# Kernel tuning notes

Hardware: AMD Instinct MI355X
Metric: run time of the kernel (lower is better)

## Reference

```python
import jax, jax.numpy as jnp
import numpy as np

EPS = 1e-4
N_ITERS = 3


def setup_inputs() -> dict:
    key = jax.random.key(0)
    k1, k2, k3, k4 = jax.random.split(key, 4)
    B, M, T, D = 8, 64, 256, 64
    M_emb = jax.random.normal(k1, (B, M, D), dtype=jnp.float32)
    Ht_n = jax.random.normal(k2, (B, T, D), dtype=jnp.float32)
    new_M_emb_init = jax.random.uniform(k3, (B, M, D), dtype=jnp.float32)
    # learned bilinear routing weights, scaled to keep exp(b) in range
    W = jax.random.normal(k4, (M, M + T, D, D), dtype=jnp.float32) * 0.01
    return {"M_emb": M_emb, "Ht_n": Ht_n, "new_M_emb_init": new_M_emb_init, "W": W}


def reference(M_emb, Ht_n, new_M_emb_init, W):
    # cat_emb: [B, M+T, D]
    cat_emb = jnp.concatenate([M_emb, Ht_n], axis=1)
    # Loop-invariant projection: u[b,i,t,d] = sum_k W[i,t,d,k] * cat_emb[b,t,k]
    # (both routing einsums contract W with cat_emb identically)
    u = jnp.einsum('itdk,btk->bitd', W, cat_emb)  # [B, M, M+T, D]
    m = new_M_emb_init  # [B, M, D]
    for _ in range(N_ITERS):
        b = jnp.einsum('bid,bitd->bit', m, u)          # routing logits
        alph = jax.nn.softmax(b, axis=-1)              # exp(b)/sum_t exp(b)
        s = jnp.tanh(jnp.einsum('bit,bitd->bid', alph, u))
        n = jnp.linalg.norm(s, axis=-1, keepdims=True) + EPS
        m = (n * n) / (1.0 + n * n) * (s / n)          # squash
    return m
```

## Files before the change

kernel.cpp:

```cpp
#include <hip/hip_runtime.h>

#define Bdim 8
#define Mdim 64
#define Tdim 256
#define MTdim 320
#define Ddim 64
#define EPSF 1e-4f

__device__ __forceinline__ void load_lds16(const void* g, void* l) {
    __builtin_amdgcn_global_load_lds(
        (const __attribute__((address_space(1))) void*)g,
        (__attribute__((address_space(3))) void*)l, 16, 0, 0);
}

__global__ __launch_bounds__(256) void u_kernel(
    const float* __restrict__ M_emb,
    const float* __restrict__ Ht,
    const float* __restrict__ W,
    float* __restrict__ u,
    int i0, int icap)
{
    const int t   = blockIdx.x;
    const int ii  = blockIdx.y;
    const int i   = i0 + ii;
    const int tid = (int)threadIdx.x;
    const int l   = tid & 63;
    const int w   = __builtin_amdgcn_readfirstlane(tid >> 6);

    __shared__ __align__(16) float wtile[64 * 64];
    __shared__ __align__(16) float catb[8 * 64];
    char* wl = (char*)wtile;
    char* cl = (char*)catb;

#pragma unroll
    for (int c = 0; c < 2; ++c) {
        const int b = 4 * c + (l >> 4);
        const float* crow = (t < Mdim)
            ? (M_emb + (((size_t)b * Mdim + t) << 6))
            : (Ht   + (((size_t)b * Tdim + (t - Mdim)) << 6));
        load_lds16((const char*)crow + (((l & 15) ^ b) * 16), cl + c * 1024);
    }

    const char* wt = (const char*)(W + (((size_t)i * MTdim + t) << 12));
#pragma unroll
    for (int s = 0; s < 4; ++s) {
        const int r   = w * 16 + s * 4 + (l >> 4);
        const int src = r * 256 + (((l & 15) ^ (r & 7)) * 16);
        load_lds16(wt + src, wl + (w * 4096 + s * 1024));
    }

    asm volatile("s_waitcnt vmcnt(0)" ::: "memory");
    __builtin_amdgcn_sched_barrier(0);

    const int d   = w * 16 + (l >> 2);
    const int bp  = l & 3;
    const int wb  = d * 256;
    const int cb0 = bp * 256;
    const int cb1 = (bp + 4) * 256;

    float a0 = 0.0f, a1 = 0.0f;
#pragma unroll
    for (int k4 = 0; k4 < 16; ++k4) {
        const float4 w4 = *reinterpret_cast<const float4*>(wl + wb  + ((k4 ^ (d & 7)) * 16));
        const float4 p  = *reinterpret_cast<const float4*>(cl + cb0 + ((k4 ^ bp) * 16));
        const float4 q  = *reinterpret_cast<const float4*>(cl + cb1 + ((k4 ^ (bp + 4)) * 16));
        a0 = fmaf(w4.x, p.x, a0); a0 = fmaf(w4.y, p.y, a0);
        a0 = fmaf(w4.z, p.z, a0); a0 = fmaf(w4.w, p.w, a0);
        a1 = fmaf(w4.x, q.x, a1); a1 = fmaf(w4.y, q.y, a1);
        a1 = fmaf(w4.z, q.z, a1); a1 = fmaf(w4.w, q.w, a1);
    }

    u[((((size_t)bp      * icap + ii) * MTdim + t) << 6) + d] = a0;
    u[((((size_t)(bp + 4)* icap + ii) * MTdim + t) << 6) + d] = a1;
}

__device__ __forceinline__ float4 shfl_xor4(float4 v, int m) {
    float4 r;
    r.x = __shfl_xor(v.x, m, 64);
    r.y = __shfl_xor(v.y, m, 64);
    r.z = __shfl_xor(v.z, m, 64);
    r.w = __shfl_xor(v.w, m, 64);
    return r;
}
__device__ __forceinline__ float4 add4(float4 a, float4 b) {
    float4 r; r.x = a.x + b.x; r.y = a.y + b.y; r.z = a.z + b.z; r.w = a.w + b.w;
    return r;
}

__global__ __launch_bounds__(320) void iter_kernel(
    const float* __restrict__ u,
    const float* __restrict__ m_init,
    float* __restrict__ out,
    int i0, int icap)
{
    const int ii   = blockIdx.x;
    const int i    = i0 + ii;
    const int b    = blockIdx.y;
    const int tid  = (int)threadIdx.x;
    const int lane = tid & 63;
    const int w    = tid >> 6;

    const float* ub = u + ((((size_t)b * icap + ii) * MTdim) << 6);

    __shared__ __align__(16) float m_lds[Ddim];
    __shared__ float wmax[5], wsum[5];
    __shared__ float partial[5 * 64];

    float4 u4[16];
    {
        const float* row = ub + ((size_t)tid << 6);
#pragma unroll
        for (int k4 = 0; k4 < 16; ++k4)
            u4[k4] = *reinterpret_cast<const float4*>(row + (k4 << 2));
    }

    if (tid < Ddim)
        m_lds[tid] = m_init[(((size_t)b * Mdim + i) << 6) + tid];
    __syncthreads();

    for (int iter = 0; iter < 3; ++iter) {
        float bt = 0.0f;
#pragma unroll
        for (int k4 = 0; k4 < 16; ++k4) {
            float4 mv = *reinterpret_cast<const float4*>(&m_lds[k4 << 2]);
            bt = fmaf(u4[k4].x, mv.x, bt);
            bt = fmaf(u4[k4].y, mv.y, bt);
            bt = fmaf(u4[k4].z, mv.z, bt);
            bt = fmaf(u4[k4].w, mv.w, bt);
        }

        float mx = bt;
#pragma unroll
        for (int off = 1; off < 64; off <<= 1)
            mx = fmaxf(mx, __shfl_xor(mx, off, 64));
        if (lane == 0) wmax[w] = mx;
        __syncthreads();
        const float bmax = fmaxf(fmaxf(fmaxf(wmax[0], wmax[1]),
                                       fmaxf(wmax[2], wmax[3])), wmax[4]);

        const float e = expf(bt - bmax);

        float sm = e;
#pragma unroll
        for (int off = 1; off < 64; off <<= 1)
            sm += __shfl_xor(sm, off, 64);
        if (lane == 0) wsum[w] = sm;

        float4 c8[8];
#pragma unroll
        for (int jj = 0; jj < 8; ++jj) {
            const bool up = (lane & 32) != 0;
            float4 keep = up ? u4[jj + 8] : u4[jj];
            float4 give = up ? u4[jj] : u4[jj + 8];
            float4 g; g.x = give.x * e; g.y = give.y * e;
                      g.z = give.z * e; g.w = give.w * e;
            float4 r = shfl_xor4(g, 32);
            float4 o;
            o.x = fmaf(keep.x, e, r.x); o.y = fmaf(keep.y, e, r.y);
            o.z = fmaf(keep.z, e, r.z); o.w = fmaf(keep.w, e, r.w);
            c8[jj] = o;
        }
        float4 c4[4];
#pragma unroll
        for (int jj = 0; jj < 4; ++jj) {
            const bool up = (lane & 16) != 0;
            float4 keep = up ? c8[jj + 4] : c8[jj];
            float4 give = up ? c8[jj] : c8[jj + 4];
            c4[jj] = add4(keep, shfl_xor4(give, 16));
        }
        float4 c2[2];
#pragma unroll
        for (int jj = 0; jj < 2; ++jj) {
            const bool up = (lane & 8) != 0;
            float4 keep = up ? c4[jj + 2] : c4[jj];
            float4 give = up ? c4[jj] : c4[jj + 2];
            c2[jj] = add4(keep, shfl_xor4(give, 8));
        }
        float4 c1;
        {
            const bool up = (lane & 4) != 0;
            float4 keep = up ? c2[1] : c2[0];
            float4 give = up ? c2[0] : c2[1];
            c1 = add4(keep, shfl_xor4(give, 4));
        }
        float p0, p1;
        {
            const bool up = (lane & 2) != 0;
            float kx = up ? c1.z : c1.x, gx = up ? c1.x : c1.z;
            float ky = up ? c1.w : c1.y, gy = up ? c1.y : c1.w;
            p0 = kx + __shfl_xor(gx, 2, 64);
            p1 = ky + __shfl_xor(gy, 2, 64);
        }
        float s_part;
        {
            const bool up = (lane & 1) != 0;
            float k1 = up ? p1 : p0, g1 = up ? p0 : p1;
            s_part = k1 + __shfl_xor(g1, 1, 64);
        }
        partial[(w << 6) + lane] = s_part;
        __syncthreads();

        if (tid < 64) {
            const float inv = 1.0f / (wsum[0] + wsum[1] + wsum[2]
                                    + wsum[3] + wsum[4]);
            float sraw = (partial[tid] + partial[64 + tid] + partial[128 + tid]
                        + partial[192 + tid] + partial[256 + tid]) * inv;
            float s  = tanhf(sraw);
            float ss = s * s;
#pragma unroll
            for (int off = 1; off < 64; off <<= 1)
                ss += __shfl_xor(ss, off, 64);
            float n = sqrtf(ss) + EPSF;
            m_lds[tid] = s * n / (1.0f + n * n);
        }
        __syncthreads();
    }

    if (tid < 64)
        out[(((size_t)b * Mdim + i) << 6) + tid] = m_lds[tid];
}

extern "C" void kernel_launch(void* const* d_in, const int* in_sizes, int n_in,
                              void* d_out, int out_size, void* d_ws, size_t ws_size,
                              hipStream_t stream) {
    const float* M_emb  = (const float*)d_in[0];
    const float* Ht     = (const float*)d_in[1];
    const float* m_init = (const float*)d_in[2];
    const float* W      = (const float*)d_in[3];
    float* out = (float*)d_out;
    float* u   = (float*)d_ws;

    const size_t per_i = (size_t)Bdim * MTdim * Ddim * sizeof(float);
    int icap = (int)(ws_size / per_i);
    if (icap > Mdim) icap = Mdim;
    if (icap < 1) icap = 1;

    for (int i0 = 0; i0 < Mdim; i0 += icap) {
        int ic = Mdim - i0 < icap ? Mdim - i0 : icap;
        dim3 g1(MTdim, ic);
        u_kernel<<<g1, dim3(256), 0, stream>>>(M_emb, Ht, W, u, i0, icap);
        dim3 g2(ic, Bdim);
        iter_kernel<<<g2, dim3(320), 0, stream>>>(u, m_init, out, i0, icap);
    }
}
```

Before: 95.08 us.

## Make u_kernel a persistent grid-stride kernel reading cat_emb from global

```diff
diff --git a/kernel.cpp b/kernel.cpp
--- a/kernel.cpp
+++ b/kernel.cpp
@@ -13,65 +13,71 @@
         (__attribute__((address_space(3))) void*)l, 16, 0, 0);
 }
 
-__global__ __launch_bounds__(256) void u_kernel(
+__global__ __launch_bounds__(256, 8) void u_kernel(
     const float* __restrict__ M_emb,
     const float* __restrict__ Ht,
     const float* __restrict__ W,
     float* __restrict__ u,
     int i0, int icap)
 {
-    const int t   = blockIdx.x;
-    const int ii  = blockIdx.y;
-    const int i   = i0 + ii;
+    const int p   = blockIdx.x;
     const int tid = (int)threadIdx.x;
     const int l   = tid & 63;
     const int w   = __builtin_amdgcn_readfirstlane(tid >> 6);
 
-    __shared__ __align__(16) float wtile[64 * 64];
-    __shared__ __align__(16) float catb[8 * 64];
-    char* wl = (char*)wtile;
-    char* cl = (char*)catb;
-
-#pragma unroll
-    for (int c = 0; c < 2; ++c) {
-        const int b = 4 * c + (l >> 4);
-        const float* crow = (t < Mdim)
-            ? (M_emb + (((size_t)b * Mdim + t) << 6))
-            : (Ht   + (((size_t)b * Tdim + (t - Mdim)) << 6));
-        load_lds16((const char*)crow + (((l & 15) ^ b) * 16), cl + c * 1024);
-    }
-
-    const char* wt = (const char*)(W + (((size_t)i * MTdim + t) << 12));
-#pragma unroll
-    for (int s = 0; s < 4; ++s) {
-        const int r   = w * 16 + s * 4 + (l >> 4);
-        const int src = r * 256 + (((l & 15) ^ (r & 7)) * 16);
-        load_lds16(wt + src, wl + (w * 4096 + s * 1024));
-    }
-
-    asm volatile("s_waitcnt vmcnt(0)" ::: "memory");
-    __builtin_amdgcn_sched_barrier(0);
+    __shared__ __align__(16) float wtile[4 * 1024];
+    char* wl = (char*)wtile + w * 4096;
 
     const int d   = w * 16 + (l >> 2);
     const int bp  = l & 3;
-    const int wb  = d * 256;
-    const int cb0 = bp * 256;
-    const int cb1 = (bp + 4) * 256;
-
-    float a0 = 0.0f, a1 = 0.0f;
-#pragma unroll
-    for (int k4 = 0; k4 < 16; ++k4) {
-        const float4 w4 = *reinterpret_cast<const float4*>(wl + wb  + ((k4 ^ (d & 7)) * 16));
-        const float4 p  = *reinterpret_cast<const float4*>(cl + cb0 + ((k4 ^ bp) * 16));
-        const float4 q  = *reinterpret_cast<const float4*>(cl + cb1 + ((k4 ^ (bp + 4)) * 16));
-        a0 = fmaf(w4.x, p.x, a0); a0 = fmaf(w4.y, p.y, a0);
-        a0 = fmaf(w4.z, p.z, a0); a0 = fmaf(w4.w, p.w, a0);
-        a1 = fmaf(w4.x, q.x, a1); a1 = fmaf(w4.y, q.y, a1);
-        a1 = fmaf(w4.z, q.z, a1); a1 = fmaf(w4.w, q.w, a1);
-    }
-
-    u[((((size_t)bp      * icap + ii) * MTdim + t) << 6) + d] = a0;
-    u[((((size_t)(bp + 4)* icap + ii) * MTdim + t) << 6) + d] = a1;
+    const int wb  = (l >> 2) * 256;
+    const int dm7 = d & 7;
+
+    const int tiles = icap * MTdim;
+
+    for (int g = 0;; ++g) {
+        const int idx = g * 2048 + p;
+        if (idx >= tiles) break;
+        const int t  = idx % MTdim;
+        const int ii = idx / MTdim;
+        const int i  = i0 + ii;
+
+        const char* wt = (const char*)(W + (((size_t)i * MTdim + t) << 12));
+#pragma unroll
+        for (int s = 0; s < 4; ++s) {
+            const int r   = w * 16 + s * 4 + (l >> 4);
+            const int src = r * 256 + (((l & 15) ^ (r & 7)) * 16);
+            load_lds16(wt + src, wl + s * 1024);
+        }
+
+        asm volatile("s_waitcnt vmcnt(0)" ::: "memory");
+        __builtin_amdgcn_sched_barrier(0);
+
+        const float* cA;
+        const float* cB;
+        if (t < Mdim) {
+            cA = M_emb + (((size_t)bp * Mdim + t) << 6);
+            cB = M_emb + (((size_t)(bp + 4) * Mdim + t) << 6);
+        } else {
+            cA = Ht + (((size_t)bp * Tdim + (t - Mdim)) << 6);
+            cB = Ht + (((size_t)(bp + 4) * Tdim + (t - Mdim)) << 6);
+        }
+
+        float a0 = 0.0f, a1 = 0.0f;
+#pragma unroll
+        for (int k4 = 0; k4 < 16; ++k4) {
+            const float4 w4 = *reinterpret_cast<const float4*>(wl + wb + ((k4 ^ dm7) * 16));
+            const float4 pc = *reinterpret_cast<const float4*>(cA + (k4 << 2));
+            const float4 qc = *reinterpret_cast<const float4*>(cB + (k4 << 2));
+            a0 = fmaf(w4.x, pc.x, a0); a0 = fmaf(w4.y, pc.y, a0);
+            a0 = fmaf(w4.z, pc.z, a0); a0 = fmaf(w4.w, pc.w, a0);
+            a1 = fmaf(w4.x, qc.x, a1); a1 = fmaf(w4.y, qc.y, a1);
+            a1 = fmaf(w4.z, qc.z, a1); a1 = fmaf(w4.w, qc.w, a1);
+        }
+
+        u[((((size_t)bp       * icap + ii) * MTdim + t) << 6) + d] = a0;
+        u[((((size_t)(bp + 4) * icap + ii) * MTdim + t) << 6) + d] = a1;
+    }
 }
 
 __device__ __forceinline__ float4 shfl_xor4(float4 v, int m) {
@@ -237,9 +243,8 @@
 
     for (int i0 = 0; i0 < Mdim; i0 += icap) {
         int ic = Mdim - i0 < icap ? Mdim - i0 : icap;
-        dim3 g1(MTdim, ic);
-        u_kernel<<<g1, dim3(256), 0, stream>>>(M_emb, Ht, W, u, i0, icap);
+        u_kernel<<<dim3(2048), dim3(256), 0, stream>>>(M_emb, Ht, W, u, i0, ic);
         dim3 g2(ic, Bdim);
-        iter_kernel<<<g2, dim3(320), 0, stream>>>(u, m_init, out, i0, icap);
-    }
-}
+        iter_kernel<<<g2, dim3(320), 0, stream>>>(u, m_init, out, i0, ic);
+    }
+}
```

After: 335.5 us. +252.8%, slower.
